# Kernel tuning notes

Hardware: AMD Instinct MI355X
Metric: run time of the kernel (lower is better)

## Reference

```python
import jax, jax.numpy as jnp
import numpy as np

N_SRC = 50000
N_DST = 50000
N_EDGES = 800000
D = 128
H = 128


def setup_inputs() -> dict:
    key = jax.random.key(0)
    ks = jax.random.split(key, 10)
    return {
        "feat_src": jax.random.normal(ks[0], (N_SRC, D), dtype=jnp.float32),
        "feat_dst": jax.random.normal(ks[1], (N_DST, D), dtype=jnp.float32),
        "W1": jax.random.normal(ks[2], (H, D), dtype=jnp.float32) * 0.05,
        "b1": jnp.zeros((H,), dtype=jnp.float32),
        "W2": jax.random.normal(ks[3], (H, 3 * D), dtype=jnp.float32) * 0.05,
        "b2": jnp.zeros((H,), dtype=jnp.float32),
        "W3": jax.random.normal(ks[4], (H, 2 * H), dtype=jnp.float32) * 0.05,
        "b3": jnp.zeros((H,), dtype=jnp.float32),
        "src_idx": jax.random.randint(ks[5], (N_EDGES,), 0, N_SRC, dtype=jnp.int32),
        "dst_idx": jax.random.randint(ks[6], (N_EDGES,), 0, N_DST, dtype=jnp.int32),
    }


def reference(feat_src, feat_dst, W1, b1, W2, b2, W3, b3, src_idx, dst_idx):
    n_dst = feat_dst.shape[0]
    # copy_u: gather source features along edges  [E, D]
    m = feat_src[src_idx]
    # fn.max -> 'max'; NOTE: source code's 'mean' is ALSO fn.max (faithful to bug)
    mx = jax.ops.segment_max(m, dst_idx, num_segments=n_dst)
    mx = jnp.where(jnp.isfinite(mx), mx, jnp.zeros_like(mx))  # zero-degree dst -> 0 (DGL convention)
    sm = jax.ops.segment_sum(m, dst_idx, num_segments=n_dst)
    agg = jnp.concatenate([mx, mx, sm], axis=1)  # [N_dst, 3D]
    z2 = agg @ W2.T + b2            # fc2
    z1 = feat_dst @ W1.T + b1       # fc1
    h = jax.nn.relu(jnp.concatenate([z2, z1], axis=1))  # [N_dst, 2H]
    out = jax.nn.relu(h @ W3.T + b3)  # fc3 = Linear + ReLU
    return out
```

## Files before the change

kernel.cpp:

```cpp
#include <hip/hip_runtime.h>
#include <math.h>

#define NDST 50000
#define NSRC 50000
#define NEDGE 800000
#define DF 128

#define NBUK 1563
#define NCH 128
#define EPC (NEDGE / NCH)
#define HN (NBUK * NCH)
#define CAP 1536

typedef __attribute__((ext_vector_type(4))) float f32x4;
typedef __attribute__((ext_vector_type(8))) short bf16x8;

__device__ __forceinline__ ushort f2bf(float f) {
    union { float f; unsigned int u; } c; c.f = f;
    unsigned int u = c.u;
    unsigned int r = (u + 0x7fffu + ((u >> 16) & 1u)) >> 16;
    return (ushort)r;
}
__device__ __forceinline__ float bflo(unsigned int u) {
    union { unsigned int u; float f; } c; c.u = u << 16; return c.f;
}
__device__ __forceinline__ float bfhi(unsigned int u) {
    union { unsigned int u; float f; } c; c.u = u & 0xffff0000u; return c.f;
}

#define PB_FS 1500
#define PB_FD 1500
#define PB_W 320
#define PB_Z 196
#define PB_TOT (PB_FS + PB_FD + PB_W + PB_Z)

__global__ void prep_all(const float* __restrict__ fs, unsigned int* __restrict__ fs_b,
                         const float* __restrict__ fd, unsigned int* __restrict__ fd_b,
                         uint4* __restrict__ hist4,
                         const float* __restrict__ W2, const float* __restrict__ W1,
                         const float* __restrict__ W3,
                         ushort* __restrict__ Wz_b, ushort* __restrict__ W1_b,
                         ushort* __restrict__ W3_b) {
    int b = blockIdx.x, tid = threadIdx.x;
    if (b < PB_FS + PB_FD) {
        const float* src = (b < PB_FS) ? fs : fd;
        unsigned int* dst = (b < PB_FS) ? fs_b : fd_b;
        int lb = (b < PB_FS) ? b : b - PB_FS;
        const int NU = NSRC * DF / 4;
        for (int u = lb * 256 + tid; u < NU; u += PB_FS * 256) {
            float4 v = ((const float4*)src)[u];
            unsigned int lo = (unsigned int)f2bf(v.x) | ((unsigned int)f2bf(v.y) << 16);
            unsigned int hi = (unsigned int)f2bf(v.z) | ((unsigned int)f2bf(v.w) << 16);
            ((uint2*)dst)[u] = make_uint2(lo, hi);
        }
    } else if (b < PB_FS + PB_FD + PB_W) {
        int i = (b - PB_FS - PB_FD) * 256 + tid;
        if (i < 128 * 256) {
            int c = i >> 8, k = i & 255;
            float v = (k < 128) ? (W2[c * 384 + k] + W2[c * 384 + 128 + k])
                                : W2[c * 384 + 128 + k];
            Wz_b[i] = f2bf(v);
        } else if (i < 128 * 256 + 128 * 128) {
            int j = i - 128 * 256;
            W1_b[j] = f2bf(W1[j]);
        } else if (i < 128 * 256 + 128 * 128 + 128 * 256) {
            int j = i - 128 * 256 - 128 * 128;
            W3_b[j] = f2bf(W3[j]);
        }
    } else {
        int i = (b - PB_FS - PB_FD - PB_W) * 256 + tid;
        if (i < HN / 4) hist4[i] = make_uint4(0, 0, 0, 0);
    }
}

__global__ void hist_k(const int* __restrict__ dst_idx, int* __restrict__ hist) {
    int e = blockIdx.x * 256 + threadIdx.x;
    if (e < NEDGE)
        atomicAdd(&hist[(dst_idx[e] >> 5) * NCH + (e / EPC)], 1);
}

__global__ void scan_bsums(const int* __restrict__ a, int* __restrict__ bsum, int n) {
    __shared__ int ws[4];
    int i = blockIdx.x * 256 + threadIdx.x;
    int v = (i < n) ? a[i] : 0;
    #pragma unroll
    for (int off = 32; off > 0; off >>= 1) v += __shfl_down(v, off, 64);
    if ((threadIdx.x & 63) == 0) ws[threadIdx.x >> 6] = v;
    __syncthreads();
    if (threadIdx.x == 0) bsum[blockIdx.x] = ws[0] + ws[1] + ws[2] + ws[3];
}

__global__ __launch_bounds__(256)
void scan_mid(const int* __restrict__ bsum, int* __restrict__ bpre, int nb) {
    __shared__ int part[256];
    int t = threadIdx.x;
    int ch = (nb + 255) / 256;
    int lo = t * ch, hi = min(nb, lo + ch);
    int s = 0;
    for (int i = lo; i < hi; ++i) s += bsum[i];
    part[t] = s;
    __syncthreads();
    for (int off = 1; off < 256; off <<= 1) {
        int v = (t >= off) ? part[t - off] : 0;
        __syncthreads();
        part[t] += v;
        __syncthreads();
    }
    int run = (t == 0) ? 0 : part[t - 1];
    for (int i = lo; i < hi; ++i) { bpre[i] = run; run += bsum[i]; }
}

__global__ __launch_bounds__(256)
void scan_final(const int* __restrict__ a, const int* __restrict__ bpre,
                int* __restrict__ out, int n) {
    __shared__ int s[256];
    int b = blockIdx.x, t = threadIdx.x;
    int i = b * 256 + t;
    int v = (i < n) ? a[i] : 0;
    s[t] = v;
    __syncthreads();
    for (int off = 1; off < 256; off <<= 1) {
        int u = (t >= off) ? s[t - off] : 0;
        __syncthreads();
        s[t] += u;
        __syncthreads();
    }
    if (i < n) out[i] = bpre[b] + s[t] - v;
}

__global__ __launch_bounds__(256)
void partition_k(const int* __restrict__ src_idx, const int* __restrict__ dst_idx,
                 const int* __restrict__ scanned, unsigned int* __restrict__ pairs) {
    __shared__ int offs_l[NBUK];
    int c = blockIdx.x, tid = threadIdx.x;
    for (int i = tid; i < NBUK; i += 256) offs_l[i] = scanned[i * NCH + c];
    __syncthreads();
    int base = c * EPC;
    for (int e = base + tid; e < base + EPC; e += 256) {
        int d = dst_idx[e];
        int pos = atomicAdd(&offs_l[d >> 5], 1);
        pairs[pos] = (unsigned int)src_idx[e] | ((unsigned int)(d & 31) << 16);
    }
}

__global__ __launch_bounds__(256)
void bucket_sort_agg(const unsigned int* __restrict__ fs_b,
                     const unsigned int* __restrict__ pairs,
                     const int* __restrict__ scanned,
                     unsigned int* __restrict__ mx_b, unsigned int* __restrict__ sm_b) {
    __shared__ int s_src[CAP];
    __shared__ int s_cnt[32], s_off[32], s_cur[32];
    int B = blockIdx.x, tid = threadIdx.x;
    int w = tid >> 6, lane = tid & 63;
    int s0 = scanned[B * NCH];
    int s1 = (B + 1 < NBUK) ? scanned[(B + 1) * NCH] : NEDGE;

    float mx0[8], mx1[8], sm0[8], sm1[8];
    #pragma unroll
    for (int j = 0; j < 8; ++j) {
        mx0[j] = -INFINITY; mx1[j] = -INFINITY; sm0[j] = 0.f; sm1[j] = 0.f;
    }

    for (int cs = s0; cs < s1; cs += CAP) {
        int n = min(CAP, s1 - cs);
        if (tid < 32) s_cnt[tid] = 0;
        __syncthreads();
        for (int i = tid; i < n; i += 256)
            atomicAdd(&s_cnt[(pairs[cs + i] >> 16) & 31u], 1);
        __syncthreads();
        if (tid < 32) {
            int v = s_cnt[tid];
            int incl = v;
            #pragma unroll
            for (int d = 1; d < 32; d <<= 1) {
                int o = __shfl_up(incl, d, 64);
                if (tid >= d) incl += o;
            }
            s_off[tid] = incl - v;
            s_cur[tid] = incl - v;
        }
        __syncthreads();
        for (int i = tid; i < n; i += 256) {
            unsigned int p = pairs[cs + i];
            int pos = atomicAdd(&s_cur[(p >> 16) & 31u], 1);
            s_src[pos] = (int)(p & 0xFFFFu);
        }
        __syncthreads();
        #pragma unroll
        for (int j = 0; j < 8; ++j) {
            int dl = w * 8 + j;
            int e = s_off[dl], eend = e + s_cnt[dl];
            for (; e + 7 < eend; e += 8) {
                unsigned int u0 = fs_b[(size_t)s_src[e] * 64 + lane];
                unsigned int u1 = fs_b[(size_t)s_src[e + 1] * 64 + lane];
                unsigned int u2 = fs_b[(size_t)s_src[e + 2] * 64 + lane];
                unsigned int u3 = fs_b[(size_t)s_src[e + 3] * 64 + lane];
                unsigned int u4 = fs_b[(size_t)s_src[e + 4] * 64 + lane];
                unsigned int u5 = fs_b[(size_t)s_src[e + 5] * 64 + lane];
                unsigned int u6 = fs_b[(size_t)s_src[e + 6] * 64 + lane];
                unsigned int u7 = fs_b[(size_t)s_src[e + 7] * 64 + lane];
                float a0 = bflo(u0), c0 = bfhi(u0);
                float a1 = bflo(u1), c1 = bfhi(u1);
                float a2 = bflo(u2), c2 = bfhi(u2);
                float a3 = bflo(u3), c3 = bfhi(u3);
                float a4 = bflo(u4), c4 = bfhi(u4);
                float a5 = bflo(u5), c5 = bfhi(u5);
                float a6 = bflo(u6), c6 = bfhi(u6);
                float a7 = bflo(u7), c7 = bfhi(u7);
                mx0[j] = fmaxf(mx0[j], fmaxf(fmaxf(fmaxf(a0, a1), fmaxf(a2, a3)),
                                             fmaxf(fmaxf(a4, a5), fmaxf(a6, a7))));
                mx1[j] = fmaxf(mx1[j], fmaxf(fmaxf(fmaxf(c0, c1), fmaxf(c2, c3)),
                                             fmaxf(fmaxf(c4, c5), fmaxf(c6, c7))));
                sm0[j] += ((a0 + a1) + (a2 + a3)) + ((a4 + a5) + (a6 + a7));
                sm1[j] += ((c0 + c1) + (c2 + c3)) + ((c4 + c5) + (c6 + c7));
            }
            for (; e + 3 < eend; e += 4) {
                unsigned int u0 = fs_b[(size_t)s_src[e] * 64 + lane];
                unsigned int u1 = fs_b[(size_t)s_src[e + 1] * 64 + lane];
                unsigned int u2 = fs_b[(size_t)s_src[e + 2] * 64 + lane];
                unsigned int u3 = fs_b[(size_t)s_src[e + 3] * 64 + lane];
                float a0 = bflo(u0), c0 = bfhi(u0);
                float a1 = bflo(u1), c1 = bfhi(u1);
                float a2 = bflo(u2), c2 = bfhi(u2);
                float a3 = bflo(u3), c3 = bfhi(u3);
                mx0[j] = fmaxf(fmaxf(fmaxf(mx0[j], a0), a1), fmaxf(a2, a3));
                mx1[j] = fmaxf(fmaxf(fmaxf(mx1[j], c0), c1), fmaxf(c2, c3));
                sm0[j] += (a0 + a1) + (a2 + a3);
                sm1[j] += (c0 + c1) + (c2 + c3);
            }
            for (; e < eend; ++e) {
                unsigned int u = fs_b[(size_t)s_src[e] * 64 + lane];
                float a = bflo(u), c = bfhi(u);
                mx0[j] = fmaxf(mx0[j], a);
                mx1[j] = fmaxf(mx1[j], c);
                sm0[j] += a;
                sm1[j] += c;
            }
        }
        __syncthreads();
    }

    int base_d = B * 32;
    #pragma unroll
    for (int j = 0; j < 8; ++j) {
        int d = base_d + w * 8 + j;
        if (d >= NDST) continue;
        float m0 = mx0[j], m1 = mx1[j];
        if (m0 == -INFINITY) m0 = 0.f;
        if (m1 == -INFINITY) m1 = 0.f;
        union { float f; unsigned int u; } c0, c1;
        c0.f = m0; c1.f = m1;
        size_t o = (size_t)d * 64 + lane;
        mx_b[o] = (c0.u >> 16) | (c1.u & 0xFFFF0000u);
        sm_b[o] = (unsigned int)f2bf(sm0[j]) | ((unsigned int)f2bf(sm1[j]) << 16);
    }
}

#define BM2 32
#define LDH 260
#define LDWS 40

__global__ __launch_bounds__(256)
void mlp_fused(const ushort* __restrict__ mxa, const ushort* __restrict__ sma,
               const ushort* __restrict__ fdb,
               const ushort* __restrict__ Wz_b, const ushort* __restrict__ W1_b,
               const ushort* __restrict__ W3_b,
               const float* __restrict__ b1, const float* __restrict__ b2,
               const float* __restrict__ b3,
               float* __restrict__ out) {
    __shared__ ushort Hs[BM2 * LDH];
    __shared__ ushort Ws[128 * LDWS];
    int tid = threadIdx.x;
    int bm = blockIdx.x * BM2;
    int wid = tid >> 6, lane = tid & 63;
    int wm = (wid & 1) * 16, wn = (wid >> 1) * 64;
    int lrow = lane & 15, lk8 = (lane >> 4) * 8;
    int rbase = (lane >> 4) * 4;

    int am0 = min(bm + wm + lrow, NDST - 1);
    int bn[4];
    #pragma unroll
    for (int ni = 0; ni < 4; ++ni) bn[ni] = wn + ni * 16 + lrow;

    int srw = tid >> 1, skw = (tid & 1) * 16;
    uint4 wr0, wr1;
    f32x4 acc[4];

#define STAGE_LOAD(Wb, K, k0) { const ushort* wp = (Wb) + (size_t)srw * (K) + (k0) + skw; \
                                wr0 = *(const uint4*)wp; wr1 = *(const uint4*)(wp + 8); }
#define STAGE_WRITE() { *(uint4*)&Ws[srw * LDWS + skw] = wr0; \
                        *(uint4*)&Ws[srw * LDWS + skw + 8] = wr1; }

    STAGE_LOAD(Wz_b, 256, 0);
    bf16x8 pA[8];
    #pragma unroll
    for (int k = 0; k < 8; ++k) {
        const ushort* ap = (k < 4) ? mxa : sma;
        int kl = ((k * 32) & 127) + lk8;
        pA[k] = *(const bf16x8*)(ap + (size_t)am0 * 128 + kl);
    }

    #pragma unroll
    for (int j = 0; j < 4; ++j) acc[j] = (f32x4){0.f, 0.f, 0.f, 0.f};
    #pragma unroll
    for (int k = 0; k < 8; ++k) {
        if (k) __syncthreads();
        STAGE_WRITE();
        __syncthreads();
        if (k < 7) { STAGE_LOAD(Wz_b, 256, (k + 1) * 32); }
        else       { STAGE_LOAD(W1_b, 128, 0); }
        #pragma unroll
        for (int ni = 0; ni < 4; ++ni) {
            bf16x8 bf = *(const bf16x8*)&Ws[bn[ni] * LDWS + lk8];
            acc[ni] = __builtin_amdgcn_mfma_f32_16x16x32_bf16(pA[k], bf, acc[ni], 0, 0, 0);
        }
    }
    bf16x8 qA[4];
    #pragma unroll
    for (int k = 0; k < 4; ++k)
        qA[k] = *(const bf16x8*)(fdb + (size_t)am0 * 128 + k * 32 + lk8);
    #pragma unroll
    for (int ni = 0; ni < 4; ++ni) {
        float bv = b2[bn[ni]];
        #pragma unroll
        for (int r = 0; r < 4; ++r)
            Hs[(wm + rbase + r) * LDH + bn[ni]] = f2bf(fmaxf(acc[ni][r] + bv, 0.f));
    }

    #pragma unroll
    for (int j = 0; j < 4; ++j) acc[j] = (f32x4){0.f, 0.f, 0.f, 0.f};
    #pragma unroll
    for (int k = 0; k < 4; ++k) {
        __syncthreads();
        STAGE_WRITE();
        __syncthreads();
        if (k < 3) { STAGE_LOAD(W1_b, 128, (k + 1) * 32); }
        else       { STAGE_LOAD(W3_b, 256, 0); }
        #pragma unroll
        for (int ni = 0; ni < 4; ++ni) {
            bf16x8 bf = *(const bf16x8*)&Ws[bn[ni] * LDWS + lk8];
            acc[ni] = __builtin_amdgcn_mfma_f32_16x16x32_bf16(qA[k], bf, acc[ni], 0, 0, 0);
        }
    }
    #pragma unroll
    for (int ni = 0; ni < 4; ++ni) {
        float bv = b1[bn[ni]];
        #pragma unroll
        for (int r = 0; r < 4; ++r)
            Hs[(wm + rbase + r) * LDH + 128 + bn[ni]] = f2bf(fmaxf(acc[ni][r] + bv, 0.f));
    }

    #pragma unroll
    for (int j = 0; j < 4; ++j) acc[j] = (f32x4){0.f, 0.f, 0.f, 0.f};
    #pragma unroll
    for (int k = 0; k < 8; ++k) {
        __syncthreads();
        STAGE_WRITE();
        __syncthreads();
        if (k < 7) { STAGE_LOAD(W3_b, 256, (k + 1) * 32); }
        bf16x8 af0 = *(const bf16x8*)&Hs[(wm + lrow) * LDH + k * 32 + lk8];
        #pragma unroll
        for (int ni = 0; ni < 4; ++ni) {
            bf16x8 bf = *(const bf16x8*)&Ws[bn[ni] * LDWS + lk8];
            acc[ni] = __builtin_amdgcn_mfma_f32_16x16x32_bf16(af0, bf, acc[ni], 0, 0, 0);
        }
    }
    #pragma unroll
    for (int ni = 0; ni < 4; ++ni) {
        float bv = b3[bn[ni]];
        #pragma unroll
        for (int r = 0; r < 4; ++r) {
            int m = bm + wm + rbase + r;
            if (m < NDST)
                out[(size_t)m * 128 + bn[ni]] = fmaxf(acc[ni][r] + bv, 0.f);
        }
    }
#undef STAGE_LOAD
#undef STAGE_WRITE
}

extern "C" void kernel_launch(void* const* d_in, const int* in_sizes, int n_in,
                              void* d_out, int out_size, void* d_ws, size_t ws_size,
                              hipStream_t stream) {
    const float* feat_src = (const float*)d_in[0];
    const float* feat_dst = (const float*)d_in[1];
    const float* W1 = (const float*)d_in[2];
    const float* b1 = (const float*)d_in[3];
    const float* W2 = (const float*)d_in[4];
    const float* b2 = (const float*)d_in[5];
    const float* W3 = (const float*)d_in[6];
    const float* b3 = (const float*)d_in[7];
    const int* src_idx = (const int*)d_in[8];
    const int* dst_idx = (const int*)d_in[9];

    float* out = (float*)d_out;

    unsigned int* fs_b = (unsigned int*)d_ws;
    unsigned int* mx_b = fs_b + (size_t)NSRC * 64;
    unsigned int* sm_b = mx_b + (size_t)NDST * 64;
    unsigned int* fd_b = sm_b + (size_t)NDST * 64;
    ushort* Wz_b = (ushort*)(fd_b + (size_t)NDST * 64);
    ushort* W1_b = Wz_b + 128 * 256;
    ushort* W3_b = W1_b + 128 * 128;
    int* hist    = (int*)(W3_b + 128 * 256);
    int* scanned = hist + HN;
    int* bsum    = scanned + HN;
    int* bpre    = bsum + 1024;
    unsigned int* pairs = (unsigned int*)(bpre + 1024);

    const int NBH = (HN + 255) / 256;

    prep_all<<<PB_TOT, 256, 0, stream>>>(
        feat_src, fs_b, feat_dst, fd_b, (uint4*)hist, W2, W1, W3, Wz_b, W1_b, W3_b);

    hist_k<<<(NEDGE + 255) / 256, 256, 0, stream>>>(dst_idx, hist);
    scan_bsums<<<NBH, 256, 0, stream>>>(hist, bsum, HN);
    scan_mid<<<1, 256, 0, stream>>>(bsum, bpre, NBH);
    scan_final<<<NBH, 256, 0, stream>>>(hist, bpre, scanned, HN);
    partition_k<<<NCH, 256, 0, stream>>>(src_idx, dst_idx, scanned, pairs);

    bucket_sort_agg<<<NBUK, 256, 0, stream>>>(fs_b, pairs, scanned, mx_b, sm_b);

    mlp_fused<<<(NDST + BM2 - 1) / BM2, 256, 0, stream>>>(
        (const ushort*)mx_b, (const ushort*)sm_b, (const ushort*)fd_b,
        Wz_b, W1_b, W3_b, b1, b2, b3, out);
}
```

Before: 145.3 us.

## Fuse fc2 GEMM into aggregation kernel and prelayout W2 into MFMA fragments

The aggregation kernel now stages its max/sum results for 32 destination rows in shared memory and immediately runs the fc2 MFMA GEMM, writing only the post-ReLU 128-wide hidden vector. The combined W2 weights are pre-packed into MFMA fragment order so each lane loads its B operand directly from global memory. This removes the mx/sm intermediate round trip, halving that traffic, and moves the fc2 stage out of the MLP kernel. In exchange the aggregation kernel uses more shared memory and registers, which may lower its occupancy, and it reads weight fragments from global memory in every block.

```diff
diff --git a/kernel.cpp b/kernel.cpp
--- a/kernel.cpp
+++ b/kernel.cpp
@@ -30,7 +30,7 @@
 
 #define PB_FS 1500
 #define PB_FD 1500
-#define PB_W 320
+#define PB_W 208
 #define PB_Z 196
 #define PB_TOT (PB_FS + PB_FD + PB_W + PB_Z)
 
@@ -39,7 +39,7 @@
                          uint4* __restrict__ hist4,
                          const float* __restrict__ W2, const float* __restrict__ W1,
                          const float* __restrict__ W3,
-                         ushort* __restrict__ Wz_b, ushort* __restrict__ W1_b,
+                         ushort* __restrict__ Wzf, ushort* __restrict__ W1_b,
                          ushort* __restrict__ W3_b) {
     int b = blockIdx.x, tid = threadIdx.x;
     if (b < PB_FS + PB_FD) {
@@ -55,16 +55,26 @@
         }
     } else if (b < PB_FS + PB_FD + PB_W) {
         int i = (b - PB_FS - PB_FD) * 256 + tid;
-        if (i < 128 * 256) {
-            int c = i >> 8, k = i & 255;
-            float v = (k < 128) ? (W2[c * 384 + k] + W2[c * 384 + 128 + k])
-                                : W2[c * 384 + 128 + k];
-            Wz_b[i] = f2bf(v);
-        } else if (i < 128 * 256 + 128 * 128) {
-            int j = i - 128 * 256;
+        if (i < 4096) {
+            int e = i, lane = e & 63, nt = (e >> 6) & 7, ks = e >> 9;
+            int n = nt * 16 + (lane & 15), kb = ks * 32 + ((lane >> 4) << 3);
+            float v[8];
+            #pragma unroll
+            for (int j = 0; j < 8; ++j) {
+                int col = kb + j;
+                v[j] = (col < 128) ? (W2[n * 384 + col] + W2[n * 384 + 128 + col])
+                                   : W2[n * 384 + 128 + col];
+            }
+            unsigned int u0 = (unsigned int)f2bf(v[0]) | ((unsigned int)f2bf(v[1]) << 16);
+            unsigned int u1 = (unsigned int)f2bf(v[2]) | ((unsigned int)f2bf(v[3]) << 16);
+            unsigned int u2 = (unsigned int)f2bf(v[4]) | ((unsigned int)f2bf(v[5]) << 16);
+            unsigned int u3 = (unsigned int)f2bf(v[6]) | ((unsigned int)f2bf(v[7]) << 16);
+            *(uint4*)(Wzf + (size_t)e * 8) = make_uint4(u0, u1, u2, u3);
+        } else if (i < 4096 + 16384) {
+            int j = i - 4096;
             W1_b[j] = f2bf(W1[j]);
-        } else if (i < 128 * 256 + 128 * 128 + 128 * 256) {
-            int j = i - 128 * 256 - 128 * 128;
+        } else if (i < 4096 + 16384 + 32768) {
+            int j = i - 4096 - 16384;
             W3_b[j] = f2bf(W3[j]);
         }
     } else {
@@ -143,13 +153,17 @@
     }
 }
 
+#define ATS 132
+
 __global__ __launch_bounds__(256)
 void bucket_sort_agg(const unsigned int* __restrict__ fs_b,
                      const unsigned int* __restrict__ pairs,
                      const int* __restrict__ scanned,
-                     unsigned int* __restrict__ mx_b, unsigned int* __restrict__ sm_b) {
+                     const ushort* __restrict__ Wzf, const float* __restrict__ b2,
+                     ushort* __restrict__ h0) {
     __shared__ int s_src[CAP];
     __shared__ int s_cnt[32], s_off[32], s_cur[32];
+    __shared__ unsigned int At[32 * ATS];
     int B = blockIdx.x, tid = threadIdx.x;
     int w = tid >> 6, lane = tid & 63;
     int s0 = scanned[B * NCH];
@@ -240,19 +254,45 @@
         __syncthreads();
     }
 
-    int base_d = B * 32;
     #pragma unroll
     for (int j = 0; j < 8; ++j) {
-        int d = base_d + w * 8 + j;
-        if (d >= NDST) continue;
-        float m0 = mx0[j], m1 = mx1[j];
-        if (m0 == -INFINITY) m0 = 0.f;
-        if (m1 == -INFINITY) m1 = 0.f;
+        int dl = w * 8 + j;
+        float m0 = (mx0[j] == -INFINITY) ? 0.f : mx0[j];
+        float m1 = (mx1[j] == -INFINITY) ? 0.f : mx1[j];
         union { float f; unsigned int u; } c0, c1;
         c0.f = m0; c1.f = m1;
-        size_t o = (size_t)d * 64 + lane;
-        mx_b[o] = (c0.u >> 16) | (c1.u & 0xFFFF0000u);
-        sm_b[o] = (unsigned int)f2bf(sm0[j]) | ((unsigned int)f2bf(sm1[j]) << 16);
+        At[dl * ATS + lane] = (c0.u >> 16) | (c1.u & 0xFFFF0000u);
+        At[dl * ATS + 64 + lane] =
+            (unsigned int)f2bf(sm0[j]) | ((unsigned int)f2bf(sm1[j]) << 16);
+    }
+    __syncthreads();
+
+    int wm = (w & 1) * 16, wn = (w >> 1) * 64;
+    int lrow = lane & 15, rbase = (lane >> 4) * 4;
+    f32x4 acc[4];
+    #pragma unroll
+    for (int ni = 0; ni < 4; ++ni) acc[ni] = (f32x4){0.f, 0.f, 0.f, 0.f};
+    #pragma unroll
+    for (int ks = 0; ks < 8; ++ks) {
+        bf16x8 af = *(const bf16x8*)&At[(wm + lrow) * ATS + ks * 16 + (lane >> 4) * 4];
+        #pragma unroll
+        for (int ni = 0; ni < 4; ++ni) {
+            bf16x8 bf = *(const bf16x8*)(Wzf +
+                ((size_t)(ks * 8 + (w >> 1) * 4 + ni) * 64 + lane) * 8);
+            acc[ni] = __builtin_amdgcn_mfma_f32_16x16x32_bf16(af, bf, acc[ni], 0, 0, 0);
+        }
+    }
+    int base_d = B * 32;
+    #pragma unroll
+    for (int ni = 0; ni < 4; ++ni) {
+        int n = wn + ni * 16 + lrow;
+        float bv = b2[n];
+        #pragma unroll
+        for (int r = 0; r < 4; ++r) {
+            int m = base_d + wm + rbase + r;
+            if (m < NDST)
+                h0[(size_t)m * 128 + n] = f2bf(fmaxf(acc[ni][r] + bv, 0.f));
+        }
     }
 }
 
@@ -261,12 +301,9 @@
 #define LDWS 40
 
 __global__ __launch_bounds__(256)
-void mlp_fused(const ushort* __restrict__ mxa, const ushort* __restrict__ sma,
-               const ushort* __restrict__ fdb,
-               const ushort* __restrict__ Wz_b, const ushort* __restrict__ W1_b,
-               const ushort* __restrict__ W3_b,
-               const float* __restrict__ b1, const float* __restrict__ b2,
-               const float* __restrict__ b3,
+void mlp_fused(const ushort* __restrict__ h0, const ushort* __restrict__ fdb,
+               const ushort* __restrict__ W1_b, const ushort* __restrict__ W3_b,
+               const float* __restrict__ b1, const float* __restrict__ b3,
                float* __restrict__ out) {
     __shared__ ushort Hs[BM2 * LDH];
     __shared__ ushort Ws[128 * LDWS];
@@ -291,47 +328,23 @@
 #define STAGE_WRITE() { *(uint4*)&Ws[srw * LDWS + skw] = wr0; \
                         *(uint4*)&Ws[srw * LDWS + skw + 8] = wr1; }
 
-    STAGE_LOAD(Wz_b, 256, 0);
-    bf16x8 pA[8];
-    #pragma unroll
-    for (int k = 0; k < 8; ++k) {
-        const ushort* ap = (k < 4) ? mxa : sma;
-        int kl = ((k * 32) & 127) + lk8;
-        pA[k] = *(const bf16x8*)(ap + (size_t)am0 * 128 + kl);
-    }
-
-    #pragma unroll
-    for (int j = 0; j < 4; ++j) acc[j] = (f32x4){0.f, 0.f, 0.f, 0.f};
-    #pragma unroll
-    for (int k = 0; k < 8; ++k) {
-        if (k) __syncthreads();
-        STAGE_WRITE();
-        __syncthreads();
-        if (k < 7) { STAGE_LOAD(Wz_b, 256, (k + 1) * 32); }
-        else       { STAGE_LOAD(W1_b, 128, 0); }
-        #pragma unroll
-        for (int ni = 0; ni < 4; ++ni) {
-            bf16x8 bf = *(const bf16x8*)&Ws[bn[ni] * LDWS + lk8];
-            acc[ni] = __builtin_amdgcn_mfma_f32_16x16x32_bf16(pA[k], bf, acc[ni], 0, 0, 0);
-        }
-    }
+    STAGE_LOAD(W1_b, 128, 0);
     bf16x8 qA[4];
     #pragma unroll
     for (int k = 0; k < 4; ++k)
         qA[k] = *(const bf16x8*)(fdb + (size_t)am0 * 128 + k * 32 + lk8);
-    #pragma unroll
-    for (int ni = 0; ni < 4; ++ni) {
-        float bv = b2[bn[ni]];
-        #pragma unroll
-        for (int r = 0; r < 4; ++r)
-            Hs[(wm + rbase + r) * LDH + bn[ni]] = f2bf(fmaxf(acc[ni][r] + bv, 0.f));
-    }
+    int u0 = tid * 2, u1 = tid * 2 + 1;
+    int hr0 = u0 >> 4, hc0 = (u0 & 15) * 8;
+    int hr1 = u1 >> 4, hc1 = (u1 & 15) * 8;
+    int hg0 = min(bm + hr0, NDST - 1), hg1 = min(bm + hr1, NDST - 1);
+    uint4 h0a = *(const uint4*)(h0 + (size_t)hg0 * 128 + hc0);
+    uint4 h0b = *(const uint4*)(h0 + (size_t)hg1 * 128 + hc1);
 
     #pragma unroll
     for (int j = 0; j < 4; ++j) acc[j] = (f32x4){0.f, 0.f, 0.f, 0.f};
     #pragma unroll
     for (int k = 0; k < 4; ++k) {
-        __syncthreads();
+        if (k) __syncthreads();
         STAGE_WRITE();
         __syncthreads();
         if (k < 3) { STAGE_LOAD(W1_b, 128, (k + 1) * 32); }
@@ -349,6 +362,8 @@
         for (int r = 0; r < 4; ++r)
             Hs[(wm + rbase + r) * LDH + 128 + bn[ni]] = f2bf(fmaxf(acc[ni][r] + bv, 0.f));
     }
+    *(uint4*)&Hs[hr0 * LDH + hc0] = h0a;
+    *(uint4*)&Hs[hr1 * LDH + hc1] = h0b;
 
     #pragma unroll
     for (int j = 0; j < 4; ++j) acc[j] = (f32x4){0.f, 0.f, 0.f, 0.f};
@@ -396,11 +411,10 @@
     float* out = (float*)d_out;
 
     unsigned int* fs_b = (unsigned int*)d_ws;
-    unsigned int* mx_b = fs_b + (size_t)NSRC * 64;
-    unsigned int* sm_b = mx_b + (size_t)NDST * 64;
-    unsigned int* fd_b = sm_b + (size_t)NDST * 64;
-    ushort* Wz_b = (ushort*)(fd_b + (size_t)NDST * 64);
-    ushort* W1_b = Wz_b + 128 * 256;
+    unsigned int* fd_b = fs_b + (size_t)NSRC * 64;
+    ushort* h0   = (ushort*)(fd_b + (size_t)NDST * 64);
+    ushort* Wzf  = h0 + (size_t)NDST * 128;
+    ushort* W1_b = Wzf + 128 * 256;
     ushort* W3_b = W1_b + 128 * 128;
     int* hist    = (int*)(W3_b + 128 * 256);
     int* scanned = hist + HN;
@@ -411,7 +425,7 @@
     const int NBH = (HN + 255) / 256;
 
     prep_all<<<PB_TOT, 256, 0, stream>>>(
-        feat_src, fs_b, feat_dst, fd_b, (uint4*)hist, W2, W1, W3, Wz_b, W1_b, W3_b);
+        feat_src, fs_b, feat_dst, fd_b, (uint4*)hist, W2, W1, W3, Wzf, W1_b, W3_b);
 
     hist_k<<<(NEDGE + 255) / 256, 256, 0, stream>>>(dst_idx, hist);
     scan_bsums<<<NBH, 256, 0, stream>>>(hist, bsum, HN);
@@ -419,9 +433,8 @@
     scan_final<<<NBH, 256, 0, stream>>>(hist, bpre, scanned, HN);
     partition_k<<<NCH, 256, 0, stream>>>(src_idx, dst_idx, scanned, pairs);
 
-    bucket_sort_agg<<<NBUK, 256, 0, stream>>>(fs_b, pairs, scanned, mx_b, sm_b);
+    bucket_sort_agg<<<NBUK, 256, 0, stream>>>(fs_b, pairs, scanned, Wzf, b2, h0);
 
     mlp_fused<<<(NDST + BM2 - 1) / BM2, 256, 0, stream>>>(
-        (const ushort*)mx_b, (const ushort*)sm_b, (const ushort*)fd_b,
-        Wz_b, W1_b, W3_b, b1, b2, b3, out);
-}
+        h0, (const ushort*)fd_b, W1_b, W3_b, b1, b3, out);
+}
```

After: 152.8 us. +5.2%, slower.
